# Performance work log

Measured on AMD Instinct MI355X. Metric: run time of the kernel, lower is better.

The kernel has to match this reference:

```python
import jax, jax.numpy as jnp
import numpy as np

B, S, H = 4, 2048, 896
NH, NKV, HD = 14, 2, 64
ROPE_THETA = 1e6


def setup_inputs() -> dict:
    key = jax.random.key(0)
    ks = jax.random.split(key, 8)
    s = 0.02
    return {
        "hidden_states": jax.random.normal(ks[0], (B, S, H), jnp.float32),
        "position_ids": jnp.arange(S, dtype=jnp.int64 if jax.config.jax_enable_x64 else jnp.int32)[None, :],
        "Wq": jax.random.normal(ks[1], (NH * HD, H), jnp.float32) * s,
        "bq": jax.random.normal(ks[2], (NH * HD,), jnp.float32) * s,
        "Wk": jax.random.normal(ks[3], (NKV * HD, H), jnp.float32) * s,
        "bk": jax.random.normal(ks[4], (NKV * HD,), jnp.float32) * s,
        "Wv": jax.random.normal(ks[5], (NKV * HD, H), jnp.float32) * s,
        "bv": jax.random.normal(ks[6], (NKV * HD,), jnp.float32) * s,
        "Wo": jax.random.normal(ks[7], (H, NH * HD), jnp.float32) * s,
    }


def _rope_cos_sin(position_ids, dtype):
    # inv_freq: [HD/2]
    inv_freq = 1.0 / (ROPE_THETA ** (jnp.arange(0, HD, 2, dtype=jnp.float32) / HD))
    # freqs: [1, S, HD/2]
    freqs = position_ids.astype(jnp.float32)[:, :, None] * inv_freq[None, None, :]
    emb = jnp.concatenate([freqs, freqs], axis=-1)  # [1, S, HD]
    return jnp.cos(emb).astype(dtype), jnp.sin(emb).astype(dtype)


def _rotate_half(x):
    x1, x2 = x[..., : HD // 2], x[..., HD // 2 :]
    return jnp.concatenate([-x2, x1], axis=-1)


def reference(hidden_states, position_ids, Wq, bq, Wk, bk, Wv, bv, Wo):
    bsz, q_len, _ = hidden_states.shape
    q = hidden_states @ Wq.T + bq  # [B,S,NH*HD]
    k = hidden_states @ Wk.T + bk  # [B,S,NKV*HD]
    v = hidden_states @ Wv.T + bv
    q = q.reshape(bsz, q_len, NH, HD).transpose(0, 2, 1, 3)    # [B,NH,S,HD]
    k = k.reshape(bsz, q_len, NKV, HD).transpose(0, 2, 1, 3)   # [B,NKV,S,HD]
    v = v.reshape(bsz, q_len, NKV, HD).transpose(0, 2, 1, 3)

    cos, sin = _rope_cos_sin(position_ids, hidden_states.dtype)
    cos, sin = cos[:, None, :, :], sin[:, None, :, :]  # broadcast over heads
    q = q * cos + _rotate_half(q) * sin
    k = k * cos + _rotate_half(k) * sin

    # GQA: repeat kv heads to NH
    n_rep = NH // NKV
    k = jnp.repeat(k, n_rep, axis=1)  # [B,NH,S,HD]
    v = jnp.repeat(v, n_rep, axis=1)

    scale = 1.0 / jnp.sqrt(jnp.asarray(HD, hidden_states.dtype))
    scores = jnp.einsum("bhqd,bhkd->bhqk", q, k) * scale  # [B,NH,S,S]
    causal = jnp.tril(jnp.ones((q_len, q_len), dtype=bool))
    scores = jnp.where(causal[None, None], scores, jnp.finfo(scores.dtype).min)
    probs = jax.nn.softmax(scores, axis=-1)
    attn = jnp.einsum("bhqk,bhkd->bhqd", probs, v)  # [B,NH,S,HD]
    attn = attn.transpose(0, 2, 1, 3).reshape(bsz, q_len, NH * HD)
    return attn @ Wo.T
```

## Files before the change

kernel.cpp:

```cpp
#include <hip/hip_runtime.h>
#include <stdint.h>

#define SB    2048
#define HID   896
#define NHEADS 14
#define NKVH  2
#define HDIM  64
#define BATCH 4
#define MROWS (BATCH*SB)
#define KVW   (NKVH*HDIM)
#define PANEL (SB*HDIM)

typedef short bfrag __attribute__((ext_vector_type(8)));
typedef float f32x4 __attribute__((ext_vector_type(4)));

__device__ __forceinline__ float b2f(unsigned short u) {
    unsigned int x = ((unsigned int)u) << 16;
    float f;
    __builtin_memcpy(&f, &x, 4);
    return f;
}
__device__ __forceinline__ unsigned short f2b(float f) {
    unsigned int x;
    __builtin_memcpy(&x, &f, 4);
    x += 0x7fffu + ((x >> 16) & 1u);
    return (unsigned short)(x >> 16);
}
__device__ __forceinline__ unsigned int pack_bf16(float lo, float hi) {
    unsigned int a, b;
    __builtin_memcpy(&a, &lo, 4);
    __builtin_memcpy(&b, &hi, 4);
    return __builtin_amdgcn_perm(b, a, 0x07060302);
}

__device__ __forceinline__ void async16(void* lds, const void* g) {
    __builtin_amdgcn_global_load_lds(
        (const __attribute__((address_space(1))) unsigned int*)g,
        (__attribute__((address_space(3))) unsigned int*)lds, 16, 0, 0);
}

#define N_HS  (MROWS*HID)
#define N_WQ  (HID*HID)
#define N_BQ  (HID)
#define N_WK  (KVW*HID)
#define N_BK  (KVW)
#define N_WO  (HID*HID)
#define C0 ((size_t)N_HS)
#define C1 (C0 + N_WQ)
#define C2 (C1 + N_BQ)
#define C3 (C2 + N_WK)
#define C4 (C3 + N_BK)
#define C5 (C4 + N_WK)
#define C6 (C5 + N_BK)
#define C7 (C6 + N_WO)

__global__ __launch_bounds__(256) void cvt_kernel(
    const float* __restrict__ a0, const float* __restrict__ a1,
    const float* __restrict__ a2, const float* __restrict__ a3,
    const float* __restrict__ a4, const float* __restrict__ a5,
    const float* __restrict__ a6, const float* __restrict__ a7,
    unsigned short* __restrict__ d0, unsigned short* __restrict__ d1,
    unsigned short* __restrict__ d2, unsigned short* __restrict__ d3,
    unsigned short* __restrict__ d4, unsigned short* __restrict__ d5,
    unsigned short* __restrict__ d6, unsigned short* __restrict__ d7)
{
    size_t i = ((size_t)blockIdx.x * 256 + threadIdx.x) * 4;
    if (i >= C7) return;
    const float* s; unsigned short* d; size_t off;
    if      (i < C0) { s = a0; d = d0; off = i; }
    else if (i < C1) { s = a1; d = d1; off = i - C0; }
    else if (i < C2) { s = a2; d = d2; off = i - C1; }
    else if (i < C3) { s = a3; d = d3; off = i - C2; }
    else if (i < C4) { s = a4; d = d4; off = i - C3; }
    else if (i < C5) { s = a5; d = d5; off = i - C4; }
    else if (i < C6) { s = a6; d = d6; off = i - C5; }
    else             { s = a7; d = d7; off = i - C6; }
    float4 v = *(const float4*)(s + off);
    ushort4 o;
    o.x = f2b(v.x); o.y = f2b(v.y); o.z = f2b(v.z); o.w = f2b(v.w);
    *(ushort4*)(d + off) = o;
}

template<int EPI>
__device__ __forceinline__ void gemm128(
    unsigned short* __restrict__ Al, unsigned short* __restrict__ Bl,
    const unsigned short* __restrict__ A, int lda,
    const unsigned short* __restrict__ W, int ldw,
    const unsigned short* __restrict__ bias,
    void* __restrict__ Cv, int ldc, int m0, int n0, int K,
    unsigned short* __restrict__ VT)
{
    const int tid  = threadIdx.x;
    const int wave = tid >> 6;
    const int lane = tid & 63;
    const int col  = lane & 15;
    const int quad = lane >> 4;
    const int wm   = (wave >> 1) * 64;
    const int wn   = (wave & 1) * 64;
    const int srow = lane >> 2;
    const int scol = (lane & 3) * 8;

    f32x4 acc[4][4] = {};

    for (int k0 = 0; k0 < K; k0 += 32) {
#pragma unroll
        for (int i = 0; i < 2; ++i) {
            const int c = wave*2 + i;
            async16(Al + c*512, A + (size_t)(m0 + c*16 + srow)*lda + k0 + scol);
            async16(Bl + c*512, W + (size_t)(n0 + c*16 + srow)*ldw + k0 + scol);
        }
        __syncthreads();
        bfrag a[4], b[4];
#pragma unroll
        for (int mb = 0; mb < 4; ++mb)
            a[mb] = *(const bfrag*)(Al + (wm + mb*16 + col)*32 + quad*8);
#pragma unroll
        for (int nb = 0; nb < 4; ++nb)
            b[nb] = *(const bfrag*)(Bl + (wn + nb*16 + col)*32 + quad*8);
#pragma unroll
        for (int mb = 0; mb < 4; ++mb)
#pragma unroll
            for (int nb = 0; nb < 4; ++nb)
                acc[mb][nb] = __builtin_amdgcn_mfma_f32_16x16x32_bf16(
                    a[mb], b[nb], acc[mb][nb], 0, 0, 0);
        __syncthreads();
    }

    if (EPI == 2) {
#pragma unroll
        for (int nb = 0; nb < 4; ++nb) {
            const int n = wn + nb*16 + col;
            const float bv = b2f(bias[n]);
            const int kvh = n >> 6;
#pragma unroll
            for (int mb = 0; mb < 4; ++mb) {
                const int m = m0 + wm + mb*16 + quad*4;
                const int bb = m >> 11, s = m & (SB-1);
                const int cc = (s >> 5) & 1;
                const int qv = (s >> 3) & 3;
                const int jb = s & 7;
                ushort4 w;
                w.x = f2b(acc[mb][nb][0] + bv);
                w.y = f2b(acc[mb][nb][1] + bv);
                w.z = f2b(acc[mb][nb][2] + bv);
                w.w = f2b(acc[mb][nb][3] + bv);
                *(ushort4*)(VT + (size_t)(bb*NKVH + kvh)*PANEL
                            + (size_t)((s >> 6)*8 + cc*4 + nb)*512
                            + (qv*16 + col)*8 + jb) = w;
            }
        }
    } else {
#pragma unroll
        for (int nb = 0; nb < 4; ++nb) {
            const int n = n0 + wn + nb*16 + col;
            const float bv = bias ? b2f(bias[n]) : 0.0f;
#pragma unroll
            for (int mb = 0; mb < 4; ++mb) {
                const size_t base = (size_t)(m0 + wm + mb*16 + quad*4) * ldc + n;
#pragma unroll
                for (int r = 0; r < 4; ++r) {
                    const float v = acc[mb][nb][r] + bv;
                    if (EPI == 1) ((float*)Cv)[base + (size_t)r * ldc] = v;
                    else ((unsigned short*)Cv)[base + (size_t)r * ldc] = f2b(v);
                }
            }
        }
    }
}

__global__ __launch_bounds__(256) void qkv_gemm(
    const unsigned short* __restrict__ hs,
    const unsigned short* __restrict__ Wq, const unsigned short* __restrict__ bq,
    const unsigned short* __restrict__ Wk, const unsigned short* __restrict__ bk,
    const unsigned short* __restrict__ Wv, const unsigned short* __restrict__ bv,
    unsigned short* __restrict__ Qw, unsigned short* __restrict__ Kw,
    unsigned short* __restrict__ Vp)
{
    __shared__ __align__(16) unsigned short Al[128*32];
    __shared__ __align__(16) unsigned short Bl[128*32];
    const int m0  = blockIdx.x * 128;
    const int seg = blockIdx.y;
    if (seg < 7)
        gemm128<0>(Al, Bl, hs, HID, Wq, HID, bq, Qw, HID, m0, seg*128, HID, nullptr);
    else if (seg == 7)
        gemm128<0>(Al, Bl, hs, HID, Wk, HID, bk, Kw, KVW, m0, 0, HID, nullptr);
    else
        gemm128<2>(Al, Bl, hs, HID, Wv, HID, bv, nullptr, 0, m0, 0, HID, Vp);
}

__global__ __launch_bounds__(256) void out_gemm(
    const unsigned short* __restrict__ Aw, const unsigned short* __restrict__ Wo,
    float* __restrict__ out)
{
    __shared__ __align__(16) unsigned short Al[128*32];
    __shared__ __align__(16) unsigned short Bl[128*32];
    gemm128<1>(Al, Bl, Aw, HID, Wo, HID, nullptr, out, HID,
               blockIdx.x * 128, blockIdx.y * 128, HID, nullptr);
}

__global__ __launch_bounds__(256) void rope_kernel(unsigned short* __restrict__ Q,
                                                   const unsigned short* __restrict__ Kw,
                                                   unsigned short* __restrict__ Kp)
{
    const int idx  = blockIdx.x * 256 + threadIdx.x;
    const int pair = idx & 31;
    const int head = (idx >> 5) & 15;
    const int m    = idx >> 9;
    const int pos  = m & (SB - 1);
    const float inv = exp2f(-(float)(2*pair) * (19.9315685693f / 64.0f));
    const float f = (float)pos * inv;
    float s, c;
    sincosf(f, &s, &c);
    if (head < NHEADS) {
        const float mul = 0.1803368801111f;
        unsigned short* base = Q + (size_t)m * HID + (size_t)head * HDIM;
        const float x1 = b2f(base[pair]);
        const float x2 = b2f(base[pair + 32]);
        base[pair]      = f2b((x1 * c - x2 * s) * mul);
        base[pair + 32] = f2b((x2 * c + x1 * s) * mul);
    } else {
        const int kvh = head - NHEADS;
        const unsigned short* src = Kw + (size_t)m * KVW + (size_t)kvh * HDIM;
        const float x1 = b2f(src[pair]);
        const float x2 = b2f(src[pair + 32]);
        const float y1 = x1 * c - x2 * s;
        const float y2 = x2 * c + x1 * s;
        const int bb = m >> 11, sq = m & (SB - 1);
        const int tile = sq >> 6, r6 = sq & 63;
        const int kb = r6 >> 4, colk = r6 & 15;
        const int quad = pair >> 3, j = pair & 7;
        unsigned short* panel = Kp + (size_t)(bb*NKVH + kvh) * PANEL;
        const size_t off0 = (size_t)(tile*8 + kb*2)*512 + (quad*16 + colk)*8 + j;
        panel[off0]       = f2b(y1);
        panel[off0 + 512] = f2b(y2);
    }
}

__global__ __launch_bounds__(64, 2) void flash_kernel(
    const unsigned short* __restrict__ Q,
    const unsigned short* __restrict__ Kp,
    const unsigned short* __restrict__ Vp,
    unsigned short* __restrict__ Aw)
{
    const int bid  = blockIdx.x;
    const int cidx = bid / 56;
    const int hb   = bid - cidx * 56;
    const int h    = hb % NHEADS;
    const int b    = hb / NHEADS;
    const int kvh  = h / 7;
    const int chunk = 63 - cidx;

    const int lane = threadIdx.x;
    const int col  = lane & 15;
    const int quad = lane >> 4;

    const int idxA = (col + ((quad & 1) << 5)) << 2;
    const int idxB = idxA + 64;
    const bool hi  = (quad >= 2);

    const unsigned short* Qb  = Q  + (size_t)b * SB * HID + (size_t)h * HDIM;
    const unsigned short* Kpp = Kp + (size_t)(b*NKVH + kvh) * PANEL;
    const unsigned short* Vpp = Vp + (size_t)(b*NKVH + kvh) * PANEL;

    bfrag ones;
#pragma unroll
    for (int jj = 0; jj < 8; ++jj) ones[jj] = (short)0x3F80;

    const int qrow  = chunk * 32;
    const int nsteps = (chunk >> 1) + 1;

    bfrag qf[2][2];
#pragma unroll
    for (int qb = 0; qb < 2; ++qb) {
        const unsigned short* qr = Qb + (size_t)(qrow + qb*16 + col) * HID;
        qf[qb][0] = *(const bfrag*)(qr + quad*8);
        qf[qb][1] = *(const bfrag*)(qr + 32 + quad*8);
    }

    f32x4 o[2][4] = {};
    f32x4 lac[2] = {};

    bfrag kc[4][2], kn[4][2];
#pragma unroll
    for (int kb = 0; kb < 4; ++kb) {
        kc[kb][0] = *(const bfrag*)(Kpp + (size_t)(kb*2 + 0)*512 + lane*8);
        kc[kb][1] = *(const bfrag*)(Kpp + (size_t)(kb*2 + 1)*512 + lane*8);
    }

    for (int step = 0; step < nsteps; ++step) {
        const size_t T = (size_t)step * 4096;
        const bool more = (step + 1 < nsteps);
        if (more) {
#pragma unroll
            for (int kb = 0; kb < 4; ++kb) {
                kn[kb][0] = *(const bfrag*)(Kpp + T + 4096 + (kb*2+0)*512 + lane*8);
                kn[kb][1] = *(const bfrag*)(Kpp + T + 4096 + (kb*2+1)*512 + lane*8);
            }
        }
        bfrag vf[2][4];
#pragma unroll
        for (int cc = 0; cc < 2; ++cc)
#pragma unroll
            for (int nb = 0; nb < 4; ++nb)
                vf[cc][nb] = *(const bfrag*)(Vpp + T + (cc*4 + nb)*512 + lane*8);

        f32x4 s[2][4];
#pragma unroll
        for (int kb = 0; kb < 4; ++kb)
#pragma unroll
            for (int qb = 0; qb < 2; ++qb) {
                f32x4 z = {};
                z = __builtin_amdgcn_mfma_f32_16x16x32_bf16(kc[kb][0], qf[qb][0], z, 0, 0, 0);
                z = __builtin_amdgcn_mfma_f32_16x16x32_bf16(kc[kb][1], qf[qb][1], z, 0, 0, 0);
                s[qb][kb] = z;
            }

        const int k0 = step * 64;
        unsigned int pk[2][4][2];
#pragma unroll
        for (int qb = 0; qb < 2; ++qb) {
            float pv[4][4];
#pragma unroll
            for (int kb = 0; kb < 4; ++kb)
#pragma unroll
                for (int r = 0; r < 4; ++r)
                    pv[kb][r] = __builtin_amdgcn_exp2f(s[qb][kb][r]);
            if (step == nsteps - 1) {
                const int q = qrow + qb*16 + col;
#pragma unroll
                for (int kb = 0; kb < 4; ++kb)
#pragma unroll
                    for (int r = 0; r < 4; ++r)
                        if (k0 + kb*16 + quad*4 + r > q) pv[kb][r] = 0.f;
            }
#pragma unroll
            for (int kb = 0; kb < 4; ++kb) {
                pk[qb][kb][0] = pack_bf16(pv[kb][0], pv[kb][1]);
                pk[qb][kb][1] = pack_bf16(pv[kb][2], pv[kb][3]);
            }
        }

#pragma unroll
        for (int cc = 0; cc < 2; ++cc)
#pragma unroll
            for (int qb = 0; qb < 2; ++qb) {
                unsigned int D[4];
#pragma unroll
                for (int jj = 0; jj < 4; ++jj) {
                    const int idx = (jj < 2) ? idxA : idxB;
                    const int t0 = __builtin_amdgcn_ds_bpermute(idx, (int)pk[qb][2*cc][jj & 1]);
                    const int t1 = __builtin_amdgcn_ds_bpermute(idx, (int)pk[qb][2*cc+1][jj & 1]);
                    D[jj] = (unsigned int)(hi ? t1 : t0);
                }
                bfrag pf;
                __builtin_memcpy(&pf, D, 16);
                lac[qb] = __builtin_amdgcn_mfma_f32_16x16x32_bf16(ones, pf, lac[qb], 0, 0, 0);
#pragma unroll
                for (int nb = 0; nb < 4; ++nb)
                    o[qb][nb] = __builtin_amdgcn_mfma_f32_16x16x32_bf16(
                        vf[cc][nb], pf, o[qb][nb], 0, 0, 0);
            }

        if (more) {
#pragma unroll
            for (int kb = 0; kb < 4; ++kb) {
                kc[kb][0] = kn[kb][0];
                kc[kb][1] = kn[kb][1];
            }
        }
    }

#pragma unroll
    for (int qb = 0; qb < 2; ++qb) {
        const float inv = 1.0f / lac[qb][0];
        const size_t row = (size_t)b * SB + qrow + qb*16 + col;
#pragma unroll
        for (int nb = 0; nb < 4; ++nb) {
            ushort4 w;
            w.x = f2b(o[qb][nb][0] * inv);
            w.y = f2b(o[qb][nb][1] * inv);
            w.z = f2b(o[qb][nb][2] * inv);
            w.w = f2b(o[qb][nb][3] * inv);
            *(ushort4*)(Aw + row * HID + h*HDIM + nb*16 + quad*4) = w;
        }
    }
}

extern "C" void kernel_launch(void* const* d_in, const int* in_sizes, int n_in,
                              void* d_out, int out_size, void* d_ws, size_t ws_size,
                              hipStream_t stream)
{
    (void)in_sizes; (void)n_in; (void)out_size; (void)ws_size;
    const float* hs_f = (const float*)d_in[0];
    const float* Wq_f = (const float*)d_in[2];
    const float* bq_f = (const float*)d_in[3];
    const float* Wk_f = (const float*)d_in[4];
    const float* bk_f = (const float*)d_in[5];
    const float* Wv_f = (const float*)d_in[6];
    const float* bv_f = (const float*)d_in[7];
    const float* Wo_f = (const float*)d_in[8];
    float* out = (float*)d_out;

    char* ws = (char*)d_ws;
    auto take = [&](size_t elems) {
        unsigned short* p = (unsigned short*)ws;
        ws += ((elems * 2 + 255) & ~(size_t)255);
        return p;
    };
    unsigned short* hs = take(N_HS);
    unsigned short* Wq = take(N_WQ);
    unsigned short* bq = take(N_BQ);
    unsigned short* Wk = take(N_WK);
    unsigned short* bk = take(N_BK);
    unsigned short* Wv = take(N_WK);
    unsigned short* bv = take(N_BK);
    unsigned short* Wo = take(N_WO);
    unsigned short* Qw = take((size_t)MROWS * HID);
    unsigned short* Kw = take((size_t)MROWS * KVW);
    unsigned short* Kp = take((size_t)MROWS * KVW);
    unsigned short* Vp = take((size_t)MROWS * KVW);
    unsigned short* Aw = take((size_t)MROWS * HID);

    cvt_kernel<<<dim3((C7/4 + 255)/256), 256, 0, stream>>>(
        hs_f, Wq_f, bq_f, Wk_f, bk_f, Wv_f, bv_f, Wo_f,
        hs, Wq, bq, Wk, bk, Wv, bv, Wo);
    qkv_gemm<<<dim3(MROWS/128, 9), 256, 0, stream>>>(hs, Wq, bq, Wk, bk, Wv, bv,
                                                     Qw, Kw, Vp);
    rope_kernel<<<dim3((MROWS*16*32)/256), 256, 0, stream>>>(Qw, Kw, Kp);
    flash_kernel<<<dim3(64*NHEADS*BATCH), 64, 0, stream>>>(Qw, Kp, Vp, Aw);
    out_gemm<<<dim3(MROWS/128, HID/128), 256, 0, stream>>>(Aw, Wo, out);
}
```

Baseline: 217.5 us.

## Split flash attention KV loop across four waves with shared-memory reduction

Each flash block now runs four wavefronts instead of one. The waves take KV tiles in an interleaved stride, so one query chunk's key range is split four ways, and their partial O and row-sum accumulators are combined through LDS before wave 0 normalizes and writes. The aim is to shorten the serial KV loop per block, which matters most for late causal chunks, and to raise the number of waves in flight. In exchange it adds a barrier and an LDS reduction, and it depends on the softmax using a fixed offset with no running max, so the partial sums can simply be added.

```diff
diff --git a/kernel.cpp b/kernel.cpp
--- a/kernel.cpp
+++ b/kernel.cpp
@@ -236,12 +236,13 @@
     }
 }
 
-__global__ __launch_bounds__(64, 2) void flash_kernel(
+__global__ __launch_bounds__(256) void flash_kernel(
     const unsigned short* __restrict__ Q,
     const unsigned short* __restrict__ Kp,
     const unsigned short* __restrict__ Vp,
     unsigned short* __restrict__ Aw)
 {
+    __shared__ float sh[3][64*35];
     const int bid  = blockIdx.x;
     const int cidx = bid / 56;
     const int hb   = bid - cidx * 56;
@@ -250,7 +251,9 @@
     const int kvh  = h / 7;
     const int chunk = 63 - cidx;
 
-    const int lane = threadIdx.x;
+    const int tid  = threadIdx.x;
+    const int w    = tid >> 6;
+    const int lane = tid & 63;
     const int col  = lane & 15;
     const int quad = lane >> 4;
 
@@ -283,18 +286,18 @@
     bfrag kc[4][2], kn[4][2];
 #pragma unroll
     for (int kb = 0; kb < 4; ++kb) {
-        kc[kb][0] = *(const bfrag*)(Kpp + (size_t)(kb*2 + 0)*512 + lane*8);
-        kc[kb][1] = *(const bfrag*)(Kpp + (size_t)(kb*2 + 1)*512 + lane*8);
-    }
-
-    for (int step = 0; step < nsteps; ++step) {
+        kc[kb][0] = *(const bfrag*)(Kpp + (size_t)w*4096 + (kb*2 + 0)*512 + lane*8);
+        kc[kb][1] = *(const bfrag*)(Kpp + (size_t)w*4096 + (kb*2 + 1)*512 + lane*8);
+    }
+
+    for (int step = w; step < nsteps; step += 4) {
         const size_t T = (size_t)step * 4096;
-        const bool more = (step + 1 < nsteps);
+        const bool more = (step + 4 < nsteps);
         if (more) {
 #pragma unroll
             for (int kb = 0; kb < 4; ++kb) {
-                kn[kb][0] = *(const bfrag*)(Kpp + T + 4096 + (kb*2+0)*512 + lane*8);
-                kn[kb][1] = *(const bfrag*)(Kpp + T + 4096 + (kb*2+1)*512 + lane*8);
+                kn[kb][0] = *(const bfrag*)(Kpp + T + 4*4096 + (kb*2+0)*512 + lane*8);
+                kn[kb][1] = *(const bfrag*)(Kpp + T + 4*4096 + (kb*2+1)*512 + lane*8);
             }
         }
         bfrag vf[2][4];
@@ -370,18 +373,47 @@
         }
     }
 
-#pragma unroll
-    for (int qb = 0; qb < 2; ++qb) {
-        const float inv = 1.0f / lac[qb][0];
-        const size_t row = (size_t)b * SB + qrow + qb*16 + col;
-#pragma unroll
-        for (int nb = 0; nb < 4; ++nb) {
-            ushort4 w;
-            w.x = f2b(o[qb][nb][0] * inv);
-            w.y = f2b(o[qb][nb][1] * inv);
-            w.z = f2b(o[qb][nb][2] * inv);
-            w.w = f2b(o[qb][nb][3] * inv);
-            *(ushort4*)(Aw + row * HID + h*HDIM + nb*16 + quad*4) = w;
+    if (w > 0) {
+        float* dst = sh[w-1] + lane*35;
+#pragma unroll
+        for (int qb = 0; qb < 2; ++qb) {
+#pragma unroll
+            for (int nb = 0; nb < 4; ++nb)
+#pragma unroll
+                for (int r = 0; r < 4; ++r)
+                    dst[qb*16 + nb*4 + r] = o[qb][nb][r];
+            dst[32 + qb] = lac[qb][0];
+        }
+    }
+    __syncthreads();
+    if (w == 0) {
+        float ltot[2] = { lac[0][0], lac[1][0] };
+#pragma unroll
+        for (int p = 0; p < 3; ++p) {
+            const float* src = sh[p] + lane*35;
+#pragma unroll
+            for (int qb = 0; qb < 2; ++qb) {
+#pragma unroll
+                for (int nb = 0; nb < 4; ++nb)
+#pragma unroll
+                    for (int r = 0; r < 4; ++r)
+                        o[qb][nb][r] += src[qb*16 + nb*4 + r];
+                ltot[qb] += src[32 + qb];
+            }
+        }
+#pragma unroll
+        for (int qb = 0; qb < 2; ++qb) {
+            const float inv = 1.0f / ltot[qb];
+            const size_t row = (size_t)b * SB + qrow + qb*16 + col;
+#pragma unroll
+            for (int nb = 0; nb < 4; ++nb) {
+                ushort4 wv;
+                wv.x = f2b(o[qb][nb][0] * inv);
+                wv.y = f2b(o[qb][nb][1] * inv);
+                wv.z = f2b(o[qb][nb][2] * inv);
+                wv.w = f2b(o[qb][nb][3] * inv);
+                *(ushort4*)(Aw + row * HID + h*HDIM + nb*16 + quad*4) = wv;
+            }
         }
     }
 }
@@ -427,6 +459,6 @@
     qkv_gemm<<<dim3(MROWS/128, 9), 256, 0, stream>>>(hs, Wq, bq, Wk, bk, Wv, bv,
                                                      Qw, Kw, Vp);
     rope_kernel<<<dim3((MROWS*16*32)/256), 256, 0, stream>>>(Qw, Kw, Kp);
-    flash_kernel<<<dim3(64*NHEADS*BATCH), 64, 0, stream>>>(Qw, Kp, Vp, Aw);
+    flash_kernel<<<dim3(64*NHEADS*BATCH), 256, 0, stream>>>(Qw, Kp, Vp, Aw);
     out_gemm<<<dim3(MROWS/128, HID/128), 256, 0, stream>>>(Aw, Wo, out);
 }
```

After: 229.3 us. 1.05x slower.
